# Kernel tuning notes

Measured on AMD Instinct MI355X. Metric: run time of the kernel, lower is better.

The kernel has to match this reference:

```python
import jax, jax.numpy as jnp
import numpy as np
from jax.scipy.special import logsumexp

WORD_DIM = 512
SCRF_DIM = 256
N_TAGS = 12
ALLOWED_SPAN = 8
START_ID = 10
STOP_ID = 11
SEQ_LEN = 768
N_SPANS = 96


def _compute_scores(h, Wl, bl, Wr, br, Gl, bgl, Gr, bgr, Wt, bt, transitions):
    # h: [1, L, D] already projected by Dense
    Lc, D = h.shape[1], h.shape[2]
    scores = jnp.zeros((1, Lc, Lc, D), h.dtype)
    diag = jnp.arange(Lc)
    ht = h
    scores = scores.at[:, diag, diag].set(ht)
    for sl in range(1, min(ALLOWED_SPAN, Lc)):
        l, r = ht[:, :-1], ht[:, 1:]
        h_hat = 4.0 * jax.nn.sigmoid(l @ Wl.T + bl + r @ Wr.T + br) - 2.0
        # exp/normalize over 3 gates == softmax over gate axis
        g = (l @ Gl.T + bgl + r @ Gr.T + bgr).reshape(1, Lc - sl, 3, D)
        wgt = jax.nn.softmax(g, axis=2)
        ht = wgt[:, :, 0] * h_hat + wgt[:, :, 1] * l + wgt[:, :, 2] * r
        scores = scores.at[:, diag[:Lc - sl], diag[sl:]].set(ht)
    tagsc = scores @ Wt.T + bt  # [1, L, L, T]
    # final[b,i,j,prev,tag] = tagsc[b,i,j,tag] + transitions[prev,tag]
    return tagsc[:, :, :, None, :] + transitions[None, None, None]


def _forward_pass(s5):
    # s5: [1, L, L, T, T]; semi-Markov forward algorithm, windows of width <= ALLOWED_SPAN
    Lc, T = s5.shape[1], s5.shape[3]
    A = ALLOWED_SPAN
    i0 = jnp.arange(1, Lc + 1)
    k = jnp.arange(A)
    p = i0[:, None] - A + k[None, :]              # candidate span-start positions [L, A]
    m = p >= 0                                    # valid window mask (istarts = max(0, i-A))
    x = s5[0][jnp.clip(p, 0), (i0 - 1)[:, None]]  # [L, A, T, T] span scores ending at i-1
    buf0 = jnp.full((A, T), -10000.0, s5.dtype).at[A - 1, START_ID].set(0.0)

    def step(buf, inp):
        xi, mi = inp
        # tmp[k, prev, tag] = score + logalpha[start, prev]
        tmp = jnp.where(mi[:, None, None], xi + buf[:, :, None], -1e30)
        na = logsumexp(tmp, axis=(0, 1))  # [T]
        return jnp.concatenate([buf[1:], na[None]], axis=0), na

    _, alphas = jax.lax.scan(step, buf0, (x, m))
    return alphas[-1, :STOP_ID].sum()


def _gold_score(s5, tags):
    Lc, T = s5.shape[1], s5.shape[3]
    gf = tags[:, :, 0] * (Lc * T * T) + tags[:, :, 1] * (T * T) + tags[:, :, 2] * T + tags[:, :, 3]
    return jnp.take_along_axis(s5.reshape(1, -1), gf, axis=1).sum()


def setup_inputs() -> dict:
    key = jax.random.key(0)
    ks = jax.random.split(key, 16)
    D, W3 = SCRF_DIM, 3 * SCRF_DIM
    s = 0.05
    def w(k, shape):
        return jax.random.normal(k, shape, dtype=jnp.float32) * s
    return {
        "feats": jax.random.normal(ks[0], (1, SEQ_LEN, WORD_DIM), dtype=jnp.float32),
        "tags": jax.random.randint(ks[1], (1, N_SPANS, 4), 0, N_TAGS),
        "Wd": w(ks[2], (D, WORD_DIM)), "bd": jnp.zeros((D,), jnp.float32),
        "Wl": w(ks[3], (D, D)), "bl": jnp.zeros((D,), jnp.float32),
        "Wr": w(ks[4], (D, D)), "br": jnp.zeros((D,), jnp.float32),
        "Gl": w(ks[5], (W3, D)), "bgl": jnp.zeros((W3,), jnp.float32),
        "Gr": w(ks[6], (W3, D)), "bgr": jnp.zeros((W3,), jnp.float32),
        "Wt": w(ks[7], (N_TAGS, D)), "bt": jnp.zeros((N_TAGS,), jnp.float32),
        "transitions": w(ks[8], (N_TAGS, N_TAGS)),
    }


def reference(feats, tags, Wd, bd, Wl, bl, Wr, br, Gl, bgl, Gr, bgr, Wt, bt, transitions):
    h = feats @ Wd.T + bd  # Dense: word_dim -> scrf_dim
    s5 = _compute_scores(h, Wl, bl, Wr, br, Gl, bgl, Gr, bgr, Wt, bt, transitions)
    gold = _gold_score(s5, tags)
    logZ = _forward_pass(s5)
    return logZ - gold
```

## Files before the change

kernel.cpp:

```cpp
#include <hip/hip_runtime.h>

typedef __attribute__((ext_vector_type(8))) short short8;
typedef __attribute__((ext_vector_type(4))) float f32x4;

__device__ __forceinline__ float bf2f(short s) {
  return __uint_as_float(((unsigned)(unsigned short)s) << 16);
}
__device__ __forceinline__ unsigned short f2bf(float f) {
  unsigned u = __float_as_uint(f);
  unsigned rounding = 0x7fffu + ((u >> 16) & 1u);
  return (unsigned short)((u + rounding) >> 16);
}

__global__ void prep_kernel(const float* __restrict__ feats, const float* __restrict__ Wd,
                            const float* __restrict__ Wl, const float* __restrict__ Wr,
                            const float* __restrict__ Gl, const float* __restrict__ Gr,
                            const float* __restrict__ bl, const float* __restrict__ br,
                            const float* __restrict__ bgl, const float* __restrict__ bgr,
                            unsigned short* __restrict__ featsB, unsigned short* __restrict__ WdB,
                            unsigned short* __restrict__ WcB, float* __restrict__ bc)
{
  int idx = blockIdx.x * 256 + threadIdx.x;
  if (idx < 393216) {
    featsB[idx] = f2bf(feats[idx]);
  } else if (idx < 524288) {
    int j = idx - 393216;
    WdB[j] = f2bf(Wd[j]);
  } else if (idx < 1048576) {
    int j = idx - 524288;
    int o = j >> 9, k = j & 511;
    float v;
    if (k < 256) v = (o < 256) ? Wl[o*256 + k] : Gl[(o-256)*256 + k];
    else { int k2 = k - 256; v = (o < 256) ? Wr[o*256 + k2] : Gr[(o-256)*256 + k2]; }
    WcB[j] = f2bf(v);
  } else if (idx < 1049600) {
    int o = idx - 1048576;
    bc[o] = (o < 256) ? bl[o] + br[o] : bgl[o-256] + bgr[o-256];
  }
}

__global__ __launch_bounds__(256) void hgemm_kernel(const unsigned short* __restrict__ A,
                                                    const unsigned short* __restrict__ W,
                                                    const float* __restrict__ bd,
                                                    unsigned short* __restrict__ C)
{
  __shared__ __align__(16) unsigned short As[64][72];
  __shared__ __align__(16) unsigned short Ws[64][72];
  int p0 = blockIdx.x * 64;
  int n0 = blockIdx.y * 64;
  int tid = threadIdx.x;
  int wave = tid >> 6, lane = tid & 63;
  f32x4 acc[4];
  #pragma unroll
  for (int i = 0; i < 4; ++i)
    #pragma unroll
    for (int j = 0; j < 4; ++j) acc[i][j] = 0.f;

  int lr = tid >> 3;
  int c8 = (tid & 7) * 8;
  for (int kt = 0; kt < 8; ++kt) {
    int kb = kt * 64;
    #pragma unroll
    for (int rr = 0; rr < 64; rr += 32) {
      int row = lr + rr;
      *(short8*)(&As[row][c8]) = *(const short8*)(A + (size_t)(p0 + row)*512 + kb + c8);
      *(short8*)(&Ws[row][c8]) = *(const short8*)(W + (size_t)(n0 + row)*512 + kb + c8);
    }
    __syncthreads();
    int q8 = (lane >> 4) * 8;
    #pragma unroll
    for (int kk = 0; kk < 2; ++kk) {
      short8 b = *(const short8*)(&Ws[wave*16 + (lane & 15)][kk*32 + q8]);
      #pragma unroll
      for (int mt = 0; mt < 4; ++mt) {
        short8 a = *(const short8*)(&As[mt*16 + (lane & 15)][kk*32 + q8]);
        acc[mt] = __builtin_amdgcn_mfma_f32_16x16x32_bf16(a, b, acc[mt], 0, 0, 0);
      }
    }
    __syncthreads();
  }
  int o = n0 + wave*16 + (lane & 15);
  float bias = bd[o];
  #pragma unroll
  for (int mt = 0; mt < 4; ++mt)
    #pragma unroll
    for (int r = 0; r < 4; ++r) {
      int row = p0 + mt*16 + (lane >> 4)*4 + r;
      C[row*256 + o] = f2bf(acc[mt][r] + bias);
    }
}

__global__ __launch_bounds__(256) void iter_kernel(const unsigned short* __restrict__ htp,
                                                   const unsigned short* __restrict__ Wc,
                                                   const float* __restrict__ bc,
                                                   unsigned short* __restrict__ htn,
                                                   int Mvalid)
{
  __shared__ __align__(16) unsigned short As[64][72];
  __shared__ __align__(16) unsigned short Ws[64][72];
  __shared__ float Cs[64][64];
  int p0 = blockIdx.x * 64;
  int n0 = blockIdx.y * 16;
  int tid = threadIdx.x;
  int wave = tid >> 6, lane = tid & 63;
  f32x4 acc[4];
  #pragma unroll
  for (int i = 0; i < 4; ++i)
    #pragma unroll
    for (int j = 0; j < 4; ++j) acc[i][j] = 0.f;

  int lr = tid >> 3;
  int c8 = (tid & 7) * 8;
  for (int kt = 0; kt < 8; ++kt) {
    int kb = kt * 64;
    int shift = kb >> 8;
    int kcol = kb & 255;
    #pragma unroll
    for (int rr = 0; rr < 64; rr += 32) {
      int row = lr + rr;
      int grow = p0 + row + shift; if (grow > 767) grow = 767;
      *(short8*)(&As[row][c8]) = *(const short8*)(htp + (size_t)grow*256 + kcol + c8);
      int o = (row >> 4)*256 + n0 + (row & 15);
      *(short8*)(&Ws[row][c8]) = *(const short8*)(Wc + (size_t)o*512 + kb + c8);
    }
    __syncthreads();
    int q8 = (lane >> 4) * 8;
    #pragma unroll
    for (int kk = 0; kk < 2; ++kk) {
      short8 b = *(const short8*)(&Ws[wave*16 + (lane & 15)][kk*32 + q8]);
      #pragma unroll
      for (int mt = 0; mt < 4; ++mt) {
        short8 a = *(const short8*)(&As[mt*16 + (lane & 15)][kk*32 + q8]);
        acc[mt] = __builtin_amdgcn_mfma_f32_16x16x32_bf16(a, b, acc[mt], 0, 0, 0);
      }
    }
    __syncthreads();
  }
  #pragma unroll
  for (int mt = 0; mt < 4; ++mt)
    #pragma unroll
    for (int r = 0; r < 4; ++r)
      Cs[mt*16 + (lane >> 4)*4 + r][wave*16 + (lane & 15)] = acc[mt][r];
  __syncthreads();

  int dl = tid & 15;
  int d = n0 + dl;
  float bz = bc[d], b0 = bc[256 + d], b1 = bc[512 + d], b2v = bc[768 + d];
  for (int pr = tid >> 4; pr < 64; pr += 16) {
    int p = p0 + pr;
    if (p >= Mvalid) continue;
    float z  = Cs[pr][dl]      + bz;
    float g0 = Cs[pr][16 + dl] + b0;
    float g1 = Cs[pr][32 + dl] + b1;
    float g2 = Cs[pr][48 + dl] + b2v;
    float l = bf2f((short)htp[p*256 + d]);
    float r = bf2f((short)htp[(p+1)*256 + d]);
    float hh = 4.f / (1.f + __expf(-z)) - 2.f;
    float mg = fmaxf(g0, fmaxf(g1, g2));
    float e0 = __expf(g0 - mg), e1 = __expf(g1 - mg), e2 = __expf(g2 - mg);
    float inv = 1.f / (e0 + e1 + e2);
    htn[p*256 + d] = f2bf((e0*hh + e1*l + e2*r) * inv);
  }
}

__global__ __launch_bounds__(128) void band_kernel(const unsigned short* __restrict__ htall,
                                                   const float* __restrict__ Wt,
                                                   const float* __restrict__ bt,
                                                   float* __restrict__ Bband,
                                                   float* __restrict__ Xn,
                                                   float* __restrict__ mu)
{
  __shared__ __align__(16) unsigned short rows[8][264];
  __shared__ float sred[96];
  __shared__ float smu;
  int i = blockIdx.x + 1;
  int tid = threadIdx.x;
  for (int q = tid; q < 256; q += 128) {
    int k = q >> 5, cc = (q & 31) * 8;
    int p = i - 8 + k, sl = 7 - k;
    short8 v;
    if (p >= 0) {
      v = *(const short8*)(htall + ((size_t)sl*768 + p)*256 + cc);
    } else {
      for (int j = 0; j < 8; ++j) v[j] = 0;
    }
    *(short8*)(&rows[k][cc]) = v;
  }
  __syncthreads();
  float res = -1e30f;
  if (tid < 96) {
    int t = tid >> 3, k = tid & 7;
    int p = i - 8 + k;
    if (p >= 0) {
      float acc = 0.f;
      for (int dch = 0; dch < 256; dch += 8) {
        float4 wa = *(const float4*)(Wt + t*256 + dch);
        float4 wb = *(const float4*)(Wt + t*256 + dch + 4);
        short8 hv = *(const short8*)(&rows[k][dch]);
        acc += wa.x*bf2f(hv[0]) + wa.y*bf2f(hv[1]) + wa.z*bf2f(hv[2]) + wa.w*bf2f(hv[3])
             + wb.x*bf2f(hv[4]) + wb.y*bf2f(hv[5]) + wb.z*bf2f(hv[6]) + wb.w*bf2f(hv[7]);
      }
      res = acc + bt[t];
    }
    Bband[(size_t)i*96 + tid] = res;
    sred[tid] = res;
  }
  __syncthreads();
  if (tid < 32) {
    float m = fmaxf(sred[tid], fmaxf(sred[tid+32], sred[tid+64]));
    #pragma unroll
    for (int off = 16; off; off >>= 1) m = fmaxf(m, __shfl_down(m, off));
    if (tid == 0) { mu[i] = m; smu = m; }
  }
  __syncthreads();
  if (tid < 96) Xn[(size_t)i*96 + tid] = __expf(res - smu);
}

__global__ __launch_bounds__(256) void chunkT_kernel(const float* __restrict__ Xn,
                                                     const float* __restrict__ mu,
                                                     const float* __restrict__ trans,
                                                     float* __restrict__ T,
                                                     float* __restrict__ C0)
{
  int chunk = blockIdx.y;
  int a = chunk * 16;
  int tid = threadIdx.x;
  if (blockIdx.x == 0 && tid == 0) C0[chunk] = 0.f;
  int wv = tid >> 6;
  int lane = tid & 63;
  int g = lane / 12;
  int t = lane - g * 12;
  int cidx = blockIdx.x * 20 + wv * 5 + g;
  bool active = (g < 5) && (cidx < 96);
  int c = active ? cidx : 95;
  int s = c / 12, tau = c - s * 12;
  float Etc[12];
  #pragma unroll
  for (int j = 0; j < 12; ++j) Etc[j] = __expf(trans[j*12 + t]);
  float NA[8], V[8];
  #pragma unroll
  for (int j = 0; j < 8; ++j) { NA[j] = 0.f; V[j] = 0.f; }
  #pragma unroll
  for (int j = 0; j < 8; ++j) if (j == s) {
    NA[j] = (t == tau) ? 1.f : 0.f;
    V[j]  = Etc[tau];
  }
  int gb = (g * 12) * 4;
  #pragma unroll
  for (int m = 1; m <= 16; ++m) {
    const float* xr = Xn + (size_t)(a + m) * 96 + t * 8;
    float4 x0 = *(const float4*)xr;
    float4 x1 = *(const float4*)(xr + 4);
    float sf = __expf(-mu[a + m]);
    float na = x0.x*V[0] + x0.y*V[1] + x0.z*V[2] + x0.w*V[3]
             + x1.x*V[4] + x1.y*V[5] + x1.z*V[6] + x1.w*V[7];
    int nai = __float_as_int(na);
    float nb[12];
    #pragma unroll
    for (int j = 0; j < 12; ++j)
      nb[j] = __int_as_float(__builtin_amdgcn_ds_bpermute(gb + j*4, nai));
    float p0 = nb[0]*Etc[0] + nb[1]*Etc[1] + nb[2]*Etc[2]  + nb[3]*Etc[3];
    float p1 = nb[4]*Etc[4] + nb[5]*Etc[5] + nb[6]*Etc[6]  + nb[7]*Etc[7];
    float p2 = nb[8]*Etc[8] + nb[9]*Etc[9] + nb[10]*Etc[10] + nb[11]*Etc[11];
    float v = (p0 + p1) + p2;
    #pragma unroll
    for (int k = 0; k < 7; ++k) { NA[k] = NA[k+1]*sf; V[k] = V[k+1]*sf; }
    NA[7] = na; V[7] = v;
  }
  if (active) {
    float* dst = T + (size_t)chunk * 9216 + c;
    #pragma unroll
    for (int j = 0; j < 8; ++j) dst[(size_t)(j*12 + t) * 96] = NA[j];
  }
}

#define TPAD 100
__global__ __launch_bounds__(256) void treemul_kernel(const float* __restrict__ Tin,
                                                      const float* __restrict__ Cin,
                                                      float* __restrict__ Tout,
                                                      float* __restrict__ Cout)
{
  __shared__ float Bs[96 * TPAD];
  __shared__ float Acs[96 * TPAD];
  __shared__ float red[8];
  int j = blockIdx.y;
  int cs = blockIdx.x * 48;
  const float* Ag = Tin + (size_t)(2*j) * 9216;
  const float* Bg = Tin + (size_t)(2*j + 1) * 9216;
  int tid = threadIdx.x;
  int wv = tid >> 6, lane = tid & 63;

  float4 av[9], bv[9];
  const float* ap = Ag + tid * 36;
  const float* bp = Bg + tid * 36;
  #pragma unroll
  for (int q = 0; q < 9; ++q) av[q] = *(const float4*)(ap + q*4);
  #pragma unroll
  for (int q = 0; q < 9; ++q) bv[q] = *(const float4*)(bp + q*4);
  float ma = 0.f, mb = 0.f;
  #pragma unroll
  for (int q = 0; q < 9; ++q) {
    ma = fmaxf(ma, fmaxf(fmaxf(av[q].x, av[q].y), fmaxf(av[q].z, av[q].w)));
    mb = fmaxf(mb, fmaxf(fmaxf(bv[q].x, bv[q].y), fmaxf(bv[q].z, bv[q].w)));
  }
  #pragma unroll
  for (int off = 32; off; off >>= 1) {
    ma = fmaxf(ma, __shfl_down(ma, off));
    mb = fmaxf(mb, __shfl_down(mb, off));
  }
  if (lane == 0) { red[wv] = ma; red[4 + wv] = mb; }
  __syncthreads();
  float fa = fmaxf(fmaxf(red[0], red[1]), fmaxf(red[2], red[3]));
  float fb = fmaxf(fmaxf(red[4], red[5]), fmaxf(red[6], red[7]));
  float ia = 1.0f / fa, ib = 1.0f / fb;

  #pragma unroll
  for (int q = 0; q < 9; ++q) {
    int e = tid*36 + q*4;
    int r = e / 96, k = e - r*96;
    float4 b = bv[q];
    b.x *= ib; b.y *= ib; b.z *= ib; b.w *= ib;
    *(float4*)&Bs[r*TPAD + k] = b;
    float4 a = av[q];
    Acs[(k+0)*TPAD + r] = a.x * ia;
    Acs[(k+1)*TPAD + r] = a.y * ia;
    Acs[(k+2)*TPAD + r] = a.z * ia;
    Acs[(k+3)*TPAD + r] = a.w * ia;
  }
  __syncthreads();

  int tr = tid >> 4, tc = tid & 15;
  int r0 = tr * 6, c0 = cs + tc * 3;
  float acc[6][3];
  #pragma unroll
  for (int i = 0; i < 6; ++i)
    #pragma unroll
    for (int m = 0; m < 3; ++m) acc[i][m] = 0.f;
  for (int k = 0; k < 96; k += 4) {
    float4 a0 = *(const float4*)&Acs[(c0+0)*TPAD + k];
    float4 a1 = *(const float4*)&Acs[(c0+1)*TPAD + k];
    float4 a2 = *(const float4*)&Acs[(c0+2)*TPAD + k];
    #pragma unroll
    for (int i = 0; i < 6; ++i) {
      float4 b = *(const float4*)&Bs[(r0+i)*TPAD + k];
      acc[i][0] += b.x*a0.x + b.y*a0.y + b.z*a0.z + b.w*a0.w;
      acc[i][1] += b.x*a1.x + b.y*a1.y + b.z*a1.z + b.w*a1.w;
      acc[i][2] += b.x*a2.x + b.y*a2.y + b.z*a2.z + b.w*a2.w;
    }
  }
  float* op = Tout + (size_t)j * 9216;
  #pragma unroll
  for (int i = 0; i < 6; ++i)
    #pragma unroll
    for (int m = 0; m < 3; ++m)
      op[(size_t)(r0+i)*96 + c0 + m] = acc[i][m];
  if (blockIdx.x == 0 && tid == 0)
    Cout[j] = Cin[2*j] + Cin[2*j + 1] + __logf(fa) + __logf(fb);
}

__global__ __launch_bounds__(256, 1) void final_kernel(const float* __restrict__ Tm,
    const float* __restrict__ Cm, const float* __restrict__ Bband,
    const float* __restrict__ mu, const float* __restrict__ trans,
    const float* __restrict__ bt, const int* __restrict__ tags,
    float* __restrict__ out)
{
  __shared__ float Qs[2][96 * TPAD];
  __shared__ float vv[4][96];
  __shared__ float red[8];
  __shared__ float redm[4];
  int tid = threadIdx.x;
  int wv = tid >> 6, lane = tid & 63;

  float4 P[9];
  const float* p0 = Tm + tid * 36;
  #pragma unroll
  for (int q = 0; q < 9; ++q) P[q] = *(const float4*)(p0 + q*4);

  float gold = 0.f;
  if (tid < 96) {
    int a = tags[tid*4+0], b = tags[tid*4+1], cc = tags[tid*4+2], d = tags[tid*4+3];
    float v = trans[cc*12 + d];
    int sl = b - a;
    if (sl >= 0 && sl < 8) v += Bband[(size_t)(b+1)*96 + d*8 + (7 - sl)];
    else v += bt[d];
    gold = v;
  }
  float mp = 0.f;
  for (int q = tid; q < 768; q += 256) mp += mu[1 + q];
  #pragma unroll
  for (int off = 32; off; off >>= 1) {
    gold += __shfl_down(gold, off);
    mp   += __shfl_down(mp, off);
  }
  if (lane == 0) { red[wv] = gold; red[4 + wv] = mp; }

  #pragma unroll
  for (int q = 0; q < 9; ++q) {
    int e = tid*36 + q*4;
    int r = e / 96, k = e - r*96;
    *(float4*)&Qs[0][r*TPAD + k] = P[q];
  }
  if (tid < 96) vv[0][tid] = (tid == 94) ? 1.f : 0.f;
  __syncthreads();
  float gold_t = red[0] + red[1] + red[2] + red[3];
  float musum  = red[4] + red[5] + red[6] + red[7];
  float Ct = Cm[0] + Cm[1] + Cm[2];

  #pragma unroll
  for (int s = 0; s < 3; ++s) {
    if (s < 2) {
      const float* pn = Tm + (size_t)(s+1)*9216 + tid*36;
      #pragma unroll
      for (int q = 0; q < 9; ++q) P[q] = *(const float4*)(pn + q*4);
    }
    float acc = 0.f;
    if (tid < 96) {
      const float* Qr = &Qs[s & 1][tid * TPAD];
      #pragma unroll
      for (int k = 0; k < 96; k += 4) {
        float4 qv = *(const float4*)(Qr + k);
        float4 zv = *(const float4*)&vv[s][k];
        acc += qv.x*zv.x + qv.y*zv.y + qv.z*zv.z + qv.w*zv.w;
      }
    }
    float am = (tid < 96) ? acc : 0.f;
    #pragma unroll
    for (int off = 32; off; off >>= 1) am = fmaxf(am, __shfl_down(am, off));
    if (lane == 0) redm[wv] = am;
    __syncthreads();
    float mx = fmaxf(fmaxf(redm[0], redm[1]), fmaxf(redm[2], redm[3]));
    Ct += __logf(mx);
    if (tid < 96) vv[s+1][tid] = acc / mx;
    if (s < 2) {
      #pragma unroll
      for (int q = 0; q < 9; ++q) {
        int e = tid*36 + q*4;
        int r = e / 96, k = e - r*96;
        *(float4*)&Qs[(s+1)&1][r*TPAD + k] = P[q];
      }
    }
    __syncthreads();
  }
  if (tid == 0) {
    float lsum = 0.f;
    #pragma unroll
    for (int t = 0; t < 11; ++t) lsum += __logf(vv[3][84 + t]);
    out[0] = lsum + 11.f * (Ct + musum) - gold_t;
  }
}

extern "C" void kernel_launch(void* const* d_in, const int* in_sizes, int n_in,
                              void* d_out, int out_size, void* d_ws, size_t ws_size,
                              hipStream_t stream)
{
  const float* feats = (const float*)d_in[0];
  const int*   tags  = (const int*)  d_in[1];
  const float* Wd    = (const float*)d_in[2];
  const float* bd    = (const float*)d_in[3];
  const float* Wl    = (const float*)d_in[4];
  const float* bl    = (const float*)d_in[5];
  const float* Wr    = (const float*)d_in[6];
  const float* br    = (const float*)d_in[7];
  const float* Gl    = (const float*)d_in[8];
  const float* bgl   = (const float*)d_in[9];
  const float* Gr    = (const float*)d_in[10];
  const float* bgr   = (const float*)d_in[11];
  const float* Wt    = (const float*)d_in[12];
  const float* bt    = (const float*)d_in[13];
  const float* trans = (const float*)d_in[14];
  float* out = (float*)d_out;

  char* ws = (char*)d_ws;
  unsigned short* featsB = (unsigned short*)(ws + 0);
  unsigned short* WdB    = (unsigned short*)(ws + 786432);
  unsigned short* WcB    = (unsigned short*)(ws + 1048576);
  float*          bc     = (float*)         (ws + 2097152);
  unsigned short* ht     = (unsigned short*)(ws + 2101248);
  float*          Bband  = (float*)         (ws + 5246976);
  float*          Xn     = (float*)         (ws + 5542272);
  float*          muv    = (float*)         (ws + 5837568);
  float*          T      = (float*)         (ws + 5841664);
  float*          Tb     = (float*)         (ws + 0);
  float*          C0     = (float*)         (ws + 1048576);
  float*          Ca     = (float*)         (ws + 1048832);
  float*          Cb     = (float*)         (ws + 1049088);

  prep_kernel<<<4100, 256, 0, stream>>>(feats, Wd, Wl, Wr, Gl, Gr, bl, br, bgl, bgr,
                                        featsB, WdB, WcB, bc);
  hgemm_kernel<<<dim3(12, 4), 256, 0, stream>>>(featsB, WdB, bd, ht);
  for (int sl = 1; sl <= 7; ++sl)
    iter_kernel<<<dim3(12, 16), 256, 0, stream>>>(ht + (size_t)(sl-1)*768*256, WcB, bc,
                                                  ht + (size_t)sl*768*256, 768 - sl);
  band_kernel<<<768, 128, 0, stream>>>(ht, Wt, bt, Bband, Xn, muv);
  chunkT_kernel<<<dim3(5, 48), 256, 0, stream>>>(Xn, muv, trans, T, C0);
  treemul_kernel<<<dim3(2, 24), 256, 0, stream>>>(T,  C0, Tb, Ca);
  treemul_kernel<<<dim3(2, 12), 256, 0, stream>>>(Tb, Ca, T,  Cb);
  treemul_kernel<<<dim3(2,  6), 256, 0, stream>>>(T,  Cb, Tb, Ca);
  treemul_kernel<<<dim3(2,  3), 256, 0, stream>>>(Tb, Ca, T,  Cb);
  final_kernel<<<1, 256, 0, stream>>>(T, Cb, Bband, muv, trans, bt, tags, out);
}
```

Baseline: 206.4 us.

## Fuse bf16 conversion into GEMM loads and use four-way tree multiplies

The fp32-to-bf16 conversion of feats and Wd moves out of the prep kernel and into the hgemm tile loads, which removes a round trip through global memory. The chain of four pairwise tree-multiply launches becomes two launches that each multiply four matrices in sequence inside one block, using shared-memory ping-pong buffers. The final kernel now does two matrix-vector products instead of three. This cuts the kernel launch count and the intermediate traffic, but the tree blocks become more serial and each block does more work, with fewer blocks to spread across the GPU.

Measured after the change: 219.2 us. +6.2%, slower.

```diff
diff --git a/kernel.cpp b/kernel.cpp
--- a/kernel.cpp
+++ b/kernel.cpp
@@ -11,38 +11,36 @@
   unsigned rounding = 0x7fffu + ((u >> 16) & 1u);
   return (unsigned short)((u + rounding) >> 16);
 }
-
-__global__ void prep_kernel(const float* __restrict__ feats, const float* __restrict__ Wd,
-                            const float* __restrict__ Wl, const float* __restrict__ Wr,
+__device__ __forceinline__ short8 cvt8(float4 a, float4 b) {
+  short8 r;
+  r[0]=(short)f2bf(a.x); r[1]=(short)f2bf(a.y); r[2]=(short)f2bf(a.z); r[3]=(short)f2bf(a.w);
+  r[4]=(short)f2bf(b.x); r[5]=(short)f2bf(b.y); r[6]=(short)f2bf(b.z); r[7]=(short)f2bf(b.w);
+  return r;
+}
+
+__global__ void prep_kernel(const float* __restrict__ Wl, const float* __restrict__ Wr,
                             const float* __restrict__ Gl, const float* __restrict__ Gr,
                             const float* __restrict__ bl, const float* __restrict__ br,
                             const float* __restrict__ bgl, const float* __restrict__ bgr,
-                            unsigned short* __restrict__ featsB, unsigned short* __restrict__ WdB,
                             unsigned short* __restrict__ WcB, float* __restrict__ bc)
 {
   int idx = blockIdx.x * 256 + threadIdx.x;
-  if (idx < 393216) {
-    featsB[idx] = f2bf(feats[idx]);
-  } else if (idx < 524288) {
-    int j = idx - 393216;
-    WdB[j] = f2bf(Wd[j]);
-  } else if (idx < 1048576) {
-    int j = idx - 524288;
-    int o = j >> 9, k = j & 511;
+  if (idx < 524288) {
+    int o = idx >> 9, k = idx & 511;
     float v;
     if (k < 256) v = (o < 256) ? Wl[o*256 + k] : Gl[(o-256)*256 + k];
     else { int k2 = k - 256; v = (o < 256) ? Wr[o*256 + k2] : Gr[(o-256)*256 + k2]; }
-    WcB[j] = f2bf(v);
-  } else if (idx < 1049600) {
-    int o = idx - 1048576;
+    WcB[idx] = f2bf(v);
+  } else if (idx < 525312) {
+    int o = idx - 524288;
     bc[o] = (o < 256) ? bl[o] + br[o] : bgl[o-256] + bgr[o-256];
   }
 }
 
-__global__ __launch_bounds__(256) void hgemm_kernel(const unsigned short* __restrict__ A,
-                                                    const unsigned short* __restrict__ W,
+__global__ __launch_bounds__(256) void hgemm_kernel(const float* __restrict__ feats,
+                                                    const float* __restrict__ Wd,
                                                     const float* __restrict__ bd,
-                                                    unsigned short* __restrict__ C)
+                                                    unsigned short* __restrict__ ht)
 {
   __shared__ __align__(16) unsigned short As[64][72];
   __shared__ __align__(16) unsigned short Ws[64][72];
@@ -50,21 +48,23 @@
   int n0 = blockIdx.y * 64;
   int tid = threadIdx.x;
   int wave = tid >> 6, lane = tid & 63;
-  f32x4 acc[4];
-  #pragma unroll
-  for (int i = 0; i < 4; ++i)
-    #pragma unroll
-    for (int j = 0; j < 4; ++j) acc[i][j] = 0.f;
-
   int lr = tid >> 3;
   int c8 = (tid & 7) * 8;
+  f32x4 acc[4];
+  #pragma unroll
+  for (int i = 0; i < 4; ++i)
+    #pragma unroll
+    for (int j = 0; j < 4; ++j) acc[i][j] = 0.f;
+
   for (int kt = 0; kt < 8; ++kt) {
     int kb = kt * 64;
     #pragma unroll
     for (int rr = 0; rr < 64; rr += 32) {
       int row = lr + rr;
-      *(short8*)(&As[row][c8]) = *(const short8*)(A + (size_t)(p0 + row)*512 + kb + c8);
-      *(short8*)(&Ws[row][c8]) = *(const short8*)(W + (size_t)(n0 + row)*512 + kb + c8);
+      const float* fp = feats + (size_t)(p0 + row)*512 + kb + c8;
+      *(short8*)(&As[row][c8]) = cvt8(*(const float4*)fp, *(const float4*)(fp + 4));
+      const float* wp = Wd + (size_t)(n0 + row)*512 + kb + c8;
+      *(short8*)(&Ws[row][c8]) = cvt8(*(const float4*)wp, *(const float4*)(wp + 4));
     }
     __syncthreads();
     int q8 = (lane >> 4) * 8;
@@ -86,7 +86,7 @@
     #pragma unroll
     for (int r = 0; r < 4; ++r) {
       int row = p0 + mt*16 + (lane >> 4)*4 + r;
-      C[row*256 + o] = f2bf(acc[mt][r] + bias);
+      ht[(size_t)row*256 + o] = f2bf(acc[mt][r] + bias);
     }
 }
 
@@ -103,14 +103,14 @@
   int n0 = blockIdx.y * 16;
   int tid = threadIdx.x;
   int wave = tid >> 6, lane = tid & 63;
-  f32x4 acc[4];
-  #pragma unroll
-  for (int i = 0; i < 4; ++i)
-    #pragma unroll
-    for (int j = 0; j < 4; ++j) acc[i][j] = 0.f;
-
   int lr = tid >> 3;
   int c8 = (tid & 7) * 8;
+  f32x4 acc[4];
+  #pragma unroll
+  for (int i = 0; i < 4; ++i)
+    #pragma unroll
+    for (int j = 0; j < 4; ++j) acc[i][j] = 0.f;
+
   for (int kt = 0; kt < 8; ++kt) {
     int kb = kt * 64;
     int shift = kb >> 8;
@@ -153,13 +153,13 @@
     float g0 = Cs[pr][16 + dl] + b0;
     float g1 = Cs[pr][32 + dl] + b1;
     float g2 = Cs[pr][48 + dl] + b2v;
-    float l = bf2f((short)htp[p*256 + d]);
-    float r = bf2f((short)htp[(p+1)*256 + d]);
+    float l = bf2f((short)htp[(size_t)p*256 + d]);
+    float r = bf2f((short)htp[(size_t)(p+1)*256 + d]);
     float hh = 4.f / (1.f + __expf(-z)) - 2.f;
     float mg = fmaxf(g0, fmaxf(g1, g2));
     float e0 = __expf(g0 - mg), e1 = __expf(g1 - mg), e2 = __expf(g2 - mg);
     float inv = 1.f / (e0 + e1 + e2);
-    htn[p*256 + d] = f2bf((e0*hh + e1*l + e2*r) * inv);
+    htn[(size_t)p*256 + d] = f2bf((e0*hh + e1*l + e2*r) * inv);
   }
 }
 
@@ -219,13 +219,11 @@
 __global__ __launch_bounds__(256) void chunkT_kernel(const float* __restrict__ Xn,
                                                      const float* __restrict__ mu,
                                                      const float* __restrict__ trans,
-                                                     float* __restrict__ T,
-                                                     float* __restrict__ C0)
+                                                     float* __restrict__ T)
 {
   int chunk = blockIdx.y;
   int a = chunk * 16;
   int tid = threadIdx.x;
-  if (blockIdx.x == 0 && tid == 0) C0[chunk] = 0.f;
   int wv = tid >> 6;
   int lane = tid & 63;
   int g = lane / 12;
@@ -274,107 +272,159 @@
   }
 }
 
-#define TPAD 100
-__global__ __launch_bounds__(256) void treemul_kernel(const float* __restrict__ Tin,
-                                                      const float* __restrict__ Cin,
-                                                      float* __restrict__ Tout,
-                                                      float* __restrict__ Cout)
-{
-  __shared__ float Bs[96 * TPAD];
-  __shared__ float Acs[96 * TPAD];
-  __shared__ float red[8];
-  int j = blockIdx.y;
-  int cs = blockIdx.x * 48;
-  const float* Ag = Tin + (size_t)(2*j) * 9216;
-  const float* Bg = Tin + (size_t)(2*j + 1) * 9216;
+#define TP 100
+__device__ __forceinline__ void mm_acc(const float* __restrict__ Bs,
+                                       const float* __restrict__ Ain,
+                                       int r0, int cl0, float acc[6][3])
+{
+  #pragma unroll
+  for (int i = 0; i < 6; ++i)
+    #pragma unroll
+    for (int m = 0; m < 3; ++m) acc[i][m] = 0.f;
+  for (int k = 0; k < 96; k += 4) {
+    float4 a0 = *(const float4*)(Ain + (cl0+0)*TP + k);
+    float4 a1 = *(const float4*)(Ain + (cl0+1)*TP + k);
+    float4 a2 = *(const float4*)(Ain + (cl0+2)*TP + k);
+    #pragma unroll
+    for (int i = 0; i < 6; ++i) {
+      float4 b = *(const float4*)(Bs + (r0+i)*TP + k);
+      acc[i][0] += b.x*a0.x + b.y*a0.y + b.z*a0.z + b.w*a0.w;
+      acc[i][1] += b.x*a1.x + b.y*a1.y + b.z*a1.z + b.w*a1.w;
+      acc[i][2] += b.x*a2.x + b.y*a2.y + b.z*a2.z + b.w*a2.w;
+    }
+  }
+}
+
+__device__ __forceinline__ float blockmax(float v, float* red, int slot) {
+  int wv = threadIdx.x >> 6, lane = threadIdx.x & 63;
+  #pragma unroll
+  for (int off = 32; off; off >>= 1) v = fmaxf(v, __shfl_down(v, off));
+  if (lane == 0) red[slot*4 + wv] = v;
+  __syncthreads();
+  return fmaxf(fmaxf(fmaxf(red[slot*4], red[slot*4+1]),
+                     fmaxf(red[slot*4+2], red[slot*4+3])), 1e-30f);
+}
+
+__device__ __forceinline__ float loadmax9(const float* M, int tid, float4* p) {
+  #pragma unroll
+  for (int q = 0; q < 9; ++q) p[q] = *(const float4*)(M + tid*36 + q*4);
+  float mx = 0.f;
+  #pragma unroll
+  for (int q = 0; q < 9; ++q)
+    mx = fmaxf(mx, fmaxf(fmaxf(p[q].x, p[q].y), fmaxf(p[q].z, p[q].w)));
+  return mx;
+}
+
+template<int WITH_CIN>
+__device__ __forceinline__ void tree_body(const float* __restrict__ Tin,
+    const float* __restrict__ Cin, float* __restrict__ Tout,
+    float* __restrict__ Cout, float* Bs, float* Rt0, float* Rt1, float* red)
+{
+  int j = blockIdx.x >> 1, slice = blockIdx.x & 1;
+  int c0 = slice * 48;
   int tid = threadIdx.x;
-  int wv = tid >> 6, lane = tid & 63;
-
-  float4 av[9], bv[9];
-  const float* ap = Ag + tid * 36;
-  const float* bp = Bg + tid * 36;
-  #pragma unroll
-  for (int q = 0; q < 9; ++q) av[q] = *(const float4*)(ap + q*4);
-  #pragma unroll
-  for (int q = 0; q < 9; ++q) bv[q] = *(const float4*)(bp + q*4);
-  float ma = 0.f, mb = 0.f;
-  #pragma unroll
-  for (int q = 0; q < 9; ++q) {
-    ma = fmaxf(ma, fmaxf(fmaxf(av[q].x, av[q].y), fmaxf(av[q].z, av[q].w)));
-    mb = fmaxf(mb, fmaxf(fmaxf(bv[q].x, bv[q].y), fmaxf(bv[q].z, bv[q].w)));
-  }
-  #pragma unroll
-  for (int off = 32; off; off >>= 1) {
-    ma = fmaxf(ma, __shfl_down(ma, off));
-    mb = fmaxf(mb, __shfl_down(mb, off));
-  }
-  if (lane == 0) { red[wv] = ma; red[4 + wv] = mb; }
-  __syncthreads();
-  float fa = fmaxf(fmaxf(red[0], red[1]), fmaxf(red[2], red[3]));
-  float fb = fmaxf(fmaxf(red[4], red[5]), fmaxf(red[6], red[7]));
-  float ia = 1.0f / fa, ib = 1.0f / fb;
-
+  const float* M0 = Tin + (size_t)(4*j    ) * 9216;
+  const float* M1 = Tin + (size_t)(4*j + 1) * 9216;
+  const float* M2 = Tin + (size_t)(4*j + 2) * 9216;
+  const float* M3 = Tin + (size_t)(4*j + 3) * 9216;
+  float4 p[9];
+
+  float fm0 = blockmax(loadmax9(M0, tid, p), red, 0);
+  float i0 = 1.f / fm0;
+  for (int q = tid; q < 4608; q += 256) {
+    int k = q / 48, cc = q - k*48;
+    Rt0[cc*TP + k] = M0[(size_t)k*96 + c0 + cc] * i0;
+  }
+  float fm1 = blockmax(loadmax9(M1, tid, p), red, 1);
+  float i1 = 1.f / fm1;
   #pragma unroll
   for (int q = 0; q < 9; ++q) {
     int e = tid*36 + q*4;
     int r = e / 96, k = e - r*96;
-    float4 b = bv[q];
-    b.x *= ib; b.y *= ib; b.z *= ib; b.w *= ib;
-    *(float4*)&Bs[r*TPAD + k] = b;
-    float4 a = av[q];
-    Acs[(k+0)*TPAD + r] = a.x * ia;
-    Acs[(k+1)*TPAD + r] = a.y * ia;
-    Acs[(k+2)*TPAD + r] = a.z * ia;
-    Acs[(k+3)*TPAD + r] = a.w * ia;
-  }
-  __syncthreads();
-
-  int tr = tid >> 4, tc = tid & 15;
-  int r0 = tr * 6, c0 = cs + tc * 3;
+    float4 v = p[q]; v.x *= i1; v.y *= i1; v.z *= i1; v.w *= i1;
+    *(float4*)&Bs[r*TP + k] = v;
+  }
+  __syncthreads();
+  int r0 = (tid >> 4) * 6, cl0 = (tid & 15) * 3;
   float acc[6][3];
+  mm_acc(Bs, Rt0, r0, cl0, acc);
   #pragma unroll
   for (int i = 0; i < 6; ++i)
     #pragma unroll
-    for (int m = 0; m < 3; ++m) acc[i][m] = 0.f;
-  for (int k = 0; k < 96; k += 4) {
-    float4 a0 = *(const float4*)&Acs[(c0+0)*TPAD + k];
-    float4 a1 = *(const float4*)&Acs[(c0+1)*TPAD + k];
-    float4 a2 = *(const float4*)&Acs[(c0+2)*TPAD + k];
-    #pragma unroll
-    for (int i = 0; i < 6; ++i) {
-      float4 b = *(const float4*)&Bs[(r0+i)*TPAD + k];
-      acc[i][0] += b.x*a0.x + b.y*a0.y + b.z*a0.z + b.w*a0.w;
-      acc[i][1] += b.x*a1.x + b.y*a1.y + b.z*a1.z + b.w*a1.w;
-      acc[i][2] += b.x*a2.x + b.y*a2.y + b.z*a2.z + b.w*a2.w;
-    }
-  }
+    for (int m = 0; m < 3; ++m) Rt1[(cl0+m)*TP + (r0+i)] = acc[i][m];
+  __syncthreads();
+
+  float fm2 = blockmax(loadmax9(M2, tid, p), red, 2);
+  float i2 = 1.f / fm2;
+  #pragma unroll
+  for (int q = 0; q < 9; ++q) {
+    int e = tid*36 + q*4;
+    int r = e / 96, k = e - r*96;
+    float4 v = p[q]; v.x *= i2; v.y *= i2; v.z *= i2; v.w *= i2;
+    *(float4*)&Bs[r*TP + k] = v;
+  }
+  __syncthreads();
+  mm_acc(Bs, Rt1, r0, cl0, acc);
+  #pragma unroll
+  for (int i = 0; i < 6; ++i)
+    #pragma unroll
+    for (int m = 0; m < 3; ++m) Rt0[(cl0+m)*TP + (r0+i)] = acc[i][m];
+  __syncthreads();
+
+  float fm3 = blockmax(loadmax9(M3, tid, p), red, 3);
+  float i3 = 1.f / fm3;
+  #pragma unroll
+  for (int q = 0; q < 9; ++q) {
+    int e = tid*36 + q*4;
+    int r = e / 96, k = e - r*96;
+    float4 v = p[q]; v.x *= i3; v.y *= i3; v.z *= i3; v.w *= i3;
+    *(float4*)&Bs[r*TP + k] = v;
+  }
+  __syncthreads();
+  mm_acc(Bs, Rt0, r0, cl0, acc);
   float* op = Tout + (size_t)j * 9216;
   #pragma unroll
   for (int i = 0; i < 6; ++i)
     #pragma unroll
     for (int m = 0; m < 3; ++m)
-      op[(size_t)(r0+i)*96 + c0 + m] = acc[i][m];
-  if (blockIdx.x == 0 && tid == 0)
-    Cout[j] = Cin[2*j] + Cin[2*j + 1] + __logf(fa) + __logf(fb);
-}
-
-__global__ __launch_bounds__(256, 1) void final_kernel(const float* __restrict__ Tm,
-    const float* __restrict__ Cm, const float* __restrict__ Bband,
-    const float* __restrict__ mu, const float* __restrict__ trans,
+      op[(size_t)(r0+i)*96 + c0 + cl0 + m] = acc[i][m];
+  if (slice == 0 && tid == 0) {
+    float base = WITH_CIN ? (Cin[4*j] + Cin[4*j+1] + Cin[4*j+2] + Cin[4*j+3]) : 0.f;
+    Cout[j] = base + __logf(fm0) + __logf(fm1) + __logf(fm2) + __logf(fm3);
+  }
+}
+
+__global__ __launch_bounds__(256) void tree1_kernel(const float* __restrict__ Tin,
+    float* __restrict__ Tout, float* __restrict__ Cout)
+{
+  __shared__ float Bs[96 * TP];
+  __shared__ float Rt0[48 * TP];
+  __shared__ float Rt1[48 * TP];
+  __shared__ float red[16];
+  tree_body<0>(Tin, nullptr, Tout, Cout, Bs, Rt0, Rt1, red);
+}
+
+__global__ __launch_bounds__(256) void tree2_kernel(const float* __restrict__ Tin,
+    const float* __restrict__ Cin, float* __restrict__ Tout, float* __restrict__ Cout)
+{
+  __shared__ float Bs[96 * TP];
+  __shared__ float Rt0[48 * TP];
+  __shared__ float Rt1[48 * TP];
+  __shared__ float red[16];
+  tree_body<1>(Tin, Cin, Tout, Cout, Bs, Rt0, Rt1, red);
+}
+
+__global__ __launch_bounds__(256, 1) void final_kernel(const float* __restrict__ Tc,
+    const float* __restrict__ Cb, const float* __restrict__ Bband,
+    const float* __restrict__ mug, const float* __restrict__ trans,
     const float* __restrict__ bt, const int* __restrict__ tags,
     float* __restrict__ out)
 {
-  __shared__ float Qs[2][96 * TPAD];
-  __shared__ float vv[4][96];
+  __shared__ float Qs[96 * TP];
+  __shared__ float v1[96], v2[96], v3[96];
   __shared__ float red[8];
-  __shared__ float redm[4];
   int tid = threadIdx.x;
   int wv = tid >> 6, lane = tid & 63;
-
-  float4 P[9];
-  const float* p0 = Tm + tid * 36;
-  #pragma unroll
-  for (int q = 0; q < 9; ++q) P[q] = *(const float4*)(p0 + q*4);
 
   float gold = 0.f;
   if (tid < 96) {
@@ -386,66 +436,51 @@
     gold = v;
   }
   float mp = 0.f;
-  for (int q = tid; q < 768; q += 256) mp += mu[1 + q];
+  for (int q = tid; q < 768; q += 256) mp += mug[1 + q];
   #pragma unroll
   for (int off = 32; off; off >>= 1) {
     gold += __shfl_down(gold, off);
     mp   += __shfl_down(mp, off);
   }
   if (lane == 0) { red[wv] = gold; red[4 + wv] = mp; }
-
-  #pragma unroll
-  for (int q = 0; q < 9; ++q) {
-    int e = tid*36 + q*4;
-    int r = e / 96, k = e - r*96;
-    *(float4*)&Qs[0][r*TPAD + k] = P[q];
-  }
-  if (tid < 96) vv[0][tid] = (tid == 94) ? 1.f : 0.f;
-  __syncthreads();
-  float gold_t = red[0] + red[1] + red[2] + red[3];
-  float musum  = red[4] + red[5] + red[6] + red[7];
-  float Ct = Cm[0] + Cm[1] + Cm[2];
-
-  #pragma unroll
-  for (int s = 0; s < 3; ++s) {
-    if (s < 2) {
-      const float* pn = Tm + (size_t)(s+1)*9216 + tid*36;
-      #pragma unroll
-      for (int q = 0; q < 9; ++q) P[q] = *(const float4*)(pn + q*4);
-    }
-    float acc = 0.f;
-    if (tid < 96) {
-      const float* Qr = &Qs[s & 1][tid * TPAD];
-      #pragma unroll
-      for (int k = 0; k < 96; k += 4) {
-        float4 qv = *(const float4*)(Qr + k);
-        float4 zv = *(const float4*)&vv[s][k];
-        acc += qv.x*zv.x + qv.y*zv.y + qv.z*zv.z + qv.w*zv.w;
-      }
-    }
-    float am = (tid < 96) ? acc : 0.f;
-    #pragma unroll
-    for (int off = 32; off; off >>= 1) am = fmaxf(am, __shfl_down(am, off));
-    if (lane == 0) redm[wv] = am;
-    __syncthreads();
-    float mx = fmaxf(fmaxf(redm[0], redm[1]), fmaxf(redm[2], redm[3]));
-    Ct += __logf(mx);
-    if (tid < 96) vv[s+1][tid] = acc / mx;
-    if (s < 2) {
-      #pragma unroll
-      for (int q = 0; q < 9; ++q) {
-        int e = tid*36 + q*4;
-        int r = e / 96, k = e - r*96;
-        *(float4*)&Qs[(s+1)&1][r*TPAD + k] = P[q];
-      }
-    }
-    __syncthreads();
-  }
+  if (tid < 96) v1[tid] = Tc[(size_t)tid*96 + 94];
+  for (int q = tid; q < 9216; q += 256) {
+    int r = q / 96, k = q - r*96;
+    Qs[r*TP + k] = Tc[9216 + q];
+  }
+  __syncthreads();
+  float goldt = red[0] + red[1] + red[2] + red[3];
+  float musum = red[4] + red[5] + red[6] + red[7];
+  if (tid < 96) {
+    float a = 0.f;
+    for (int k = 0; k < 96; k += 4) {
+      float4 qv = *(const float4*)&Qs[tid*TP + k];
+      float4 zv = *(const float4*)&v1[k];
+      a += qv.x*zv.x + qv.y*zv.y + qv.z*zv.z + qv.w*zv.w;
+    }
+    v2[tid] = a;
+  }
+  __syncthreads();
+  for (int q = tid; q < 9216; q += 256) {
+    int r = q / 96, k = q - r*96;
+    Qs[r*TP + k] = Tc[18432 + q];
+  }
+  __syncthreads();
+  if (tid < 96) {
+    float a = 0.f;
+    for (int k = 0; k < 96; k += 4) {
+      float4 qv = *(const float4*)&Qs[tid*TP + k];
+      float4 zv = *(const float4*)&v2[k];
+      a += qv.x*zv.x + qv.y*zv.y + qv.z*zv.z + qv.w*zv.w;
+    }
+    v3[tid] = a;
+  }
+  __syncthreads();
   if (tid == 0) {
-    float lsum = 0.f;
-    #pragma unroll
-    for (int t = 0; t < 11; ++t) lsum += __logf(vv[3][84 + t]);
-    out[0] = lsum + 11.f * (Ct + musum) - gold_t;
+    float ls = 0.f;
+    #pragma unroll
+    for (int t = 0; t < 11; ++t) ls += __logf(v3[84 + t]);
+    out[0] = ls + 11.f * (Cb[0] + Cb[1] + Cb[2] + musum) - goldt;
   }
 }
 
@@ -471,31 +506,26 @@
   float* out = (float*)d_out;
 
   char* ws = (char*)d_ws;
-  unsigned short* featsB = (unsigned short*)(ws + 0);
-  unsigned short* WdB    = (unsigned short*)(ws + 786432);
-  unsigned short* WcB    = (unsigned short*)(ws + 1048576);
-  float*          bc     = (float*)         (ws + 2097152);
-  unsigned short* ht     = (unsigned short*)(ws + 2101248);
-  float*          Bband  = (float*)         (ws + 5246976);
-  float*          Xn     = (float*)         (ws + 5542272);
-  float*          muv    = (float*)         (ws + 5837568);
-  float*          T      = (float*)         (ws + 5841664);
-  float*          Tb     = (float*)         (ws + 0);
-  float*          C0     = (float*)         (ws + 1048576);
-  float*          Ca     = (float*)         (ws + 1048832);
-  float*          Cb     = (float*)         (ws + 1049088);
-
-  prep_kernel<<<4100, 256, 0, stream>>>(feats, Wd, Wl, Wr, Gl, Gr, bl, br, bgl, bgr,
-                                        featsB, WdB, WcB, bc);
-  hgemm_kernel<<<dim3(12, 4), 256, 0, stream>>>(featsB, WdB, bd, ht);
+  unsigned short* WcB   = (unsigned short*)(ws + 0);
+  float*          bc    = (float*)(ws + 1048576);
+  unsigned short* ht    = (unsigned short*)(ws + 1052672);
+  float*          Bband = (float*)(ws + 4198400);
+  float*          Xn    = (float*)(ws + 4493696);
+  float*          mug   = (float*)(ws + 4788992);
+  float*          T     = (float*)(ws + 4792320);
+  float*          Tb    = (float*)(ws + 6561792);
+  float*          Tc    = (float*)(ws + 7004160);
+  float*          Ca    = (float*)(ws + 7114752);
+  float*          Cb    = (float*)(ws + 7114816);
+
+  prep_kernel<<<2052, 256, 0, stream>>>(Wl, Wr, Gl, Gr, bl, br, bgl, bgr, WcB, bc);
+  hgemm_kernel<<<dim3(12, 4), 256, 0, stream>>>(feats, Wd, bd, ht);
   for (int sl = 1; sl <= 7; ++sl)
-    iter_kernel<<<dim3(12, 16), 256, 0, stream>>>(ht + (size_t)(sl-1)*768*256, WcB, bc,
-                                                  ht + (size_t)sl*768*256, 768 - sl);
-  band_kernel<<<768, 128, 0, stream>>>(ht, Wt, bt, Bband, Xn, muv);
-  chunkT_kernel<<<dim3(5, 48), 256, 0, stream>>>(Xn, muv, trans, T, C0);
-  treemul_kernel<<<dim3(2, 24), 256, 0, stream>>>(T,  C0, Tb, Ca);
-  treemul_kernel<<<dim3(2, 12), 256, 0, stream>>>(Tb, Ca, T,  Cb);
-  treemul_kernel<<<dim3(2,  6), 256, 0, stream>>>(T,  Cb, Tb, Ca);
-  treemul_kernel<<<dim3(2,  3), 256, 0, stream>>>(Tb, Ca, T,  Cb);
-  final_kernel<<<1, 256, 0, stream>>>(T, Cb, Bband, muv, trans, bt, tags, out);
-}
+    iter_kernel<<<dim3(12, 16), 256, 0, stream>>>(ht + (size_t)(sl-1)*196608, WcB, bc,
+                                                  ht + (size_t)sl*196608, 768 - sl);
+  band_kernel<<<768, 128, 0, stream>>>(ht, Wt, bt, Bband, Xn, mug);
+  chunkT_kernel<<<dim3(5, 48), 256, 0, stream>>>(Xn, mug, trans, T);
+  tree1_kernel<<<24, 256, 0, stream>>>(T, Tb, Ca);
+  tree2_kernel<<<6, 256, 0, stream>>>(Tb, Ca, Tc, Cb);
+  final_kernel<<<1, 256, 0, stream>>>(Tc, Cb, Bband, mug, trans, bt, tags, out);
+}
```
